# Performance work log

Hardware: AMD Instinct MI355X
Metric: run time of the kernel (lower is better)

## Reference

```python
import jax, jax.numpy as jnp
import numpy as np

EMBED_DIM = 1024
NUM_HEADS = 16
HEAD_DIM = EMBED_DIM // NUM_HEADS


def setup_inputs() -> dict:
    key = jax.random.key(0)
    ks = jax.random.split(key, 9)
    B, N, D = 2, 2048, EMBED_DIM
    s = 1.0 / np.sqrt(D)
    return {
        "x": jax.random.normal(ks[0], (B, N, D), jnp.float32),
        "Wq": jax.random.normal(ks[1], (D, D), jnp.float32) * s,
        "bq": jax.random.normal(ks[2], (D,), jnp.float32) * 0.01,
        "Wk": jax.random.normal(ks[3], (D, D), jnp.float32) * s,
        "bk": jax.random.normal(ks[4], (D,), jnp.float32) * 0.01,
        "Wv": jax.random.normal(ks[5], (D, D), jnp.float32) * s,
        "bv": jax.random.normal(ks[6], (D,), jnp.float32) * 0.01,
        "Wo": jax.random.normal(ks[7], (D, D), jnp.float32) * s,
        "bo": jax.random.normal(ks[8], (D,), jnp.float32) * 0.01,
    }


def reference(x, Wq, bq, Wk, bk, Wv, bv, Wo, bo):
    B, N, D = x.shape
    H, Hd = NUM_HEADS, HEAD_DIM
    # QKV projections (Linear: x @ W^T + b), split heads -> [B, H, N, Hd]
    q = (x @ Wq.T + bq).reshape(B, N, H, Hd).transpose(0, 2, 1, 3)
    k = (x @ Wk.T + bk).reshape(B, N, H, Hd).transpose(0, 2, 1, 3)
    v = (x @ Wv.T + bv).reshape(B, N, H, Hd).transpose(0, 2, 1, 3)
    scale = 1.0 / np.sqrt(Hd)
    scores = jnp.einsum("bhqd,bhkd->bhqk", q, k) * scale  # [B,H,N,N]
    attn = jax.nn.softmax(scores.astype(jnp.float32), axis=-1).astype(scores.dtype)
    out = jnp.einsum("bhqk,bhkd->bhqd", attn, v)  # [B,H,N,Hd]
    out = out.transpose(0, 2, 1, 3).reshape(B, N, D)
    return out @ Wo.T + bo
```

## Files before the change

kernel.cpp:

```cpp
#include <hip/hip_runtime.h>
#include <hip/hip_bf16.h>

typedef __attribute__((ext_vector_type(8))) short short8;
typedef __attribute__((ext_vector_type(4))) float f32x4;
typedef __attribute__((ext_vector_type(4))) unsigned short us4;

static __device__ __forceinline__ unsigned short f2bf(float f) {
    union { float f; unsigned u; } v; v.f = f;
    unsigned r = (v.u + 0x7FFFu + ((v.u >> 16) & 1u)) >> 16;
    return (unsigned short)r;
}
static __device__ __forceinline__ unsigned short f2bf_fast(float f) {
    union { float f; unsigned u; } v; v.f = f;
    return (unsigned short)((v.u + 0x8000u) >> 16);
}

#if __has_builtin(__builtin_amdgcn_exp2f)
#define EXP2(x) __builtin_amdgcn_exp2f(x)
#else
#define EXP2(x) exp2f(x)
#endif

static __device__ __forceinline__ void gld16(const unsigned short* g, unsigned short* l) {
    __builtin_amdgcn_global_load_lds(
        (const __attribute__((address_space(1))) void*)g,
        (__attribute__((address_space(3))) void*)l, 16, 0, 0);
}

__global__ __launch_bounds__(256) void convert_all(
    const float* __restrict__ x,  const float* __restrict__ wq,
    const float* __restrict__ wk, const float* __restrict__ wv,
    const float* __restrict__ wo, const float* __restrict__ bq,
    const float* __restrict__ bk, const float* __restrict__ bv,
    unsigned short* __restrict__ xbf, unsigned short* __restrict__ wqkv,
    unsigned short* __restrict__ wobf, float* __restrict__ bqkv)
{
    const int NX4 = (4096 * 1024) / 4;
    const int NW4 = (1024 * 1024) / 4;
    int i = blockIdx.x * 256 + threadIdx.x;
    if (i < NX4) {
        float4 v = ((const float4*)x)[i];
        us4 o = { f2bf(v.x), f2bf(v.y), f2bf(v.z), f2bf(v.w) };
        ((us4*)xbf)[i] = o;
    } else if (i < NX4 + 3 * NW4) {
        int j = i - NX4;
        const float* src = (j < NW4) ? wq + 4 * j
                         : (j < 2 * NW4) ? wk + 4 * (j - NW4)
                         : wv + 4 * (j - 2 * NW4);
        float4 v = *(const float4*)src;
        us4 o = { f2bf(v.x), f2bf(v.y), f2bf(v.z), f2bf(v.w) };
        ((us4*)wqkv)[j] = o;
    } else if (i < NX4 + 4 * NW4) {
        int j = i - NX4 - 3 * NW4;
        float4 v = ((const float4*)wo)[j];
        us4 o = { f2bf(v.x), f2bf(v.y), f2bf(v.z), f2bf(v.w) };
        ((us4*)wobf)[j] = o;
    } else if (i < NX4 + 4 * NW4 + 768) {
        int j = i - NX4 - 4 * NW4;
        const float* src = (j < 256) ? bq + 4 * j
                         : (j < 512) ? bk + 4 * (j - 256)
                         : bv + 4 * (j - 512);
        ((float4*)bqkv)[j] = *(const float4*)src;
    }
}

template <int MODE>
__global__ __launch_bounds__(256) void gemm_bt(
    const unsigned short* __restrict__ A, const unsigned short* __restrict__ B,
    const float* __restrict__ bias,
    unsigned short* __restrict__ Qb, unsigned short* __restrict__ Kb,
    unsigned short* __restrict__ Vtb, float* __restrict__ Cout, int Mtiles)
{
    __shared__ __attribute__((aligned(16))) unsigned short As[128 * 72];
    __shared__ __attribute__((aligned(16))) unsigned short Bs[128 * 72];
    const int tid = threadIdx.x, lane = tid & 63, wave = tid >> 6;
    const int bm = blockIdx.x % Mtiles, bn = blockIdx.x / Mtiles;
    const int m0 = bm * 128, n0 = bn * 128;
    const int wr = wave >> 1, wc = wave & 1;
    const int lo = lane & 15, g = lane >> 4;

    f32x4 acc[4][4];
#pragma unroll
    for (int i = 0; i < 4; ++i)
#pragma unroll
        for (int j = 0; j < 4; ++j) acc[i][j] = (f32x4){0.f, 0.f, 0.f, 0.f};

    for (int kt = 0; kt < 16; ++kt) {
        const int k0 = kt * 64;
#pragma unroll
        for (int p = 0; p < 4; ++p) {
            int idx = p * 256 + tid;
            int row = idx >> 3, c8 = (idx & 7) << 3;
            uint4 va;
            if (MODE == 0) {
                va = *(const uint4*)(A + (size_t)(m0 + row) * 1024 + k0 + c8);
            } else {
                int gr = m0 + row, b = gr >> 11, n = gr & 2047;
                va = *(const uint4*)(A + ((size_t)((b << 4) + kt) * 2048 + n) * 64 + c8);
            }
            *(uint4*)&As[row * 72 + c8] = va;
            uint4 vb = *(const uint4*)(B + (size_t)(n0 + row) * 1024 + k0 + c8);
            *(uint4*)&Bs[row * 72 + c8] = vb;
        }
        __syncthreads();
        short8 af[4][2], bf[4][2];
#pragma unroll
        for (int i = 0; i < 4; ++i)
#pragma unroll
            for (int kc = 0; kc < 2; ++kc) {
                af[i][kc] = *(const short8*)&As[(wr * 64 + i * 16 + lo) * 72 + kc * 32 + g * 8];
                bf[i][kc] = *(const short8*)&Bs[(wc * 64 + i * 16 + lo) * 72 + kc * 32 + g * 8];
            }
#pragma unroll
        for (int kc = 0; kc < 2; ++kc)
#pragma unroll
            for (int i = 0; i < 4; ++i)
#pragma unroll
                for (int j = 0; j < 4; ++j)
                    acc[i][j] = __builtin_amdgcn_mfma_f32_16x16x32_bf16(
                        af[i][kc], bf[j][kc], acc[i][j], 0, 0, 0);
        __syncthreads();
    }

#pragma unroll
    for (int i = 0; i < 4; ++i)
#pragma unroll
        for (int j = 0; j < 4; ++j)
#pragma unroll
            for (int r = 0; r < 4; ++r) {
                int gr = m0 + wr * 64 + i * 16 + g * 4 + r;
                int gc = n0 + wc * 64 + j * 16 + lo;
                float v = acc[i][j][r] + bias[gc];
                if (MODE == 0) {
                    int b = gr >> 11, n = gr & 2047;
                    int sect = gc >> 10, d = gc & 1023, h = d >> 6, hd = d & 63;
                    if (sect == 0)
                        Qb[((size_t)((b << 4) + h) * 2048 + n) * 64 + hd] = f2bf(v);
                    else if (sect == 1)
                        Kb[((size_t)((b << 4) + h) * 2048 + n) * 64 + hd] = f2bf(v);
                    else
                        Vtb[((size_t)((b << 4) + h) * 64 + hd) * 2048 + n] = f2bf(v);
                } else {
                    Cout[(size_t)gr * 1024 + gc] = v;
                }
            }
}

__global__ __launch_bounds__(256, 2) void attn_kernel(
    const unsigned short* __restrict__ Qb, const unsigned short* __restrict__ Kb,
    const unsigned short* __restrict__ Vtb, unsigned short* __restrict__ Ob)
{
    __shared__ __attribute__((aligned(16))) unsigned short Ks[128 * 64];
    __shared__ __attribute__((aligned(16))) unsigned short Vs[64 * 128];
    __shared__ __attribute__((aligned(16))) unsigned short Ps[4 * 32 * 136];
    const int tid = threadIdx.x, lane = tid & 63, wave = tid >> 6;
    const int lo = lane & 15, g = lane >> 4;
    const int bh = blockIdx.x >> 4, qt = blockIdx.x & 15;
    const size_t base = (size_t)bh * (2048 * 64);
    const int q0w = qt * 128 + wave * 32;
    const float k2 = 0.125f * 1.44269504f;

    short8 aq[2][2];
#pragma unroll
    for (int rb = 0; rb < 2; ++rb) {
        const unsigned short* qp = Qb + base + (size_t)(q0w + rb * 16 + lo) * 64 + g * 8;
        aq[rb][0] = *(const short8*)qp;
        aq[rb][1] = *(const short8*)(qp + 32);
    }
    f32x4 o[2][4];
    float l[2][4];
#pragma unroll
    for (int rb = 0; rb < 2; ++rb) {
#pragma unroll
        for (int c = 0; c < 4; ++c) o[rb][c] = (f32x4){0.f, 0.f, 0.f, 0.f};
#pragma unroll
        for (int r = 0; r < 4; ++r) l[rb][r] = 0.f;
    }
    unsigned short* myP = Ps + wave * (32 * 136);
    const unsigned short* Kg0 = Kb + base;
    const unsigned short* Vg0 = Vtb + (size_t)bh * (64 * 2048);

    for (int kt = 0; kt < 16; ++kt) {
        const int k0 = kt * 128;
#pragma unroll
        for (int i = 0; i < 4; ++i) {
            int off = (wave * 4 + i) * 512 + lane * 8;
            gld16(Kg0 + (size_t)k0 * 64 + off, &Ks[off]);
        }
#pragma unroll
        for (int i = 0; i < 4; ++i) {
            int off = (wave * 4 + i) * 512 + lane * 8;
            int row = off >> 7, col = off & 127;
            gld16(Vg0 + (size_t)row * 2048 + k0 + col, &Vs[off]);
        }
        __syncthreads();

        f32x4 s[2][8];
#pragma unroll
        for (int ct = 0; ct < 8; ++ct) {
            short8 b0 = *(const short8*)&Ks[(ct * 16 + lo) * 64 + g * 8];
            short8 b1 = *(const short8*)&Ks[(ct * 16 + lo) * 64 + 32 + g * 8];
#pragma unroll
            for (int rb = 0; rb < 2; ++rb) {
                f32x4 z = (f32x4){0.f, 0.f, 0.f, 0.f};
                s[rb][ct] = __builtin_amdgcn_mfma_f32_16x16x32_bf16(aq[rb][0], b0, z, 0, 0, 0);
                s[rb][ct] = __builtin_amdgcn_mfma_f32_16x16x32_bf16(aq[rb][1], b1, s[rb][ct], 0, 0, 0);
            }
        }
#pragma unroll
        for (int rb = 0; rb < 2; ++rb)
#pragma unroll
            for (int ct = 0; ct < 8; ++ct)
#pragma unroll
                for (int r = 0; r < 4; ++r) {
                    float p = EXP2(s[rb][ct][r] * k2);
                    l[rb][r] += p;
                    myP[(rb * 16 + g * 4 + r) * 136 + ct * 16 + lo] = f2bf_fast(p);
                }
#pragma unroll
        for (int kc = 0; kc < 4; ++kc) {
            short8 ap0 = *(const short8*)&myP[lo * 136 + kc * 32 + g * 8];
            short8 ap1 = *(const short8*)&myP[(16 + lo) * 136 + kc * 32 + g * 8];
#pragma unroll
            for (int c = 0; c < 4; ++c) {
                short8 bv = *(const short8*)&Vs[(c * 16 + lo) * 128 + kc * 32 + g * 8];
                o[0][c] = __builtin_amdgcn_mfma_f32_16x16x32_bf16(ap0, bv, o[0][c], 0, 0, 0);
                o[1][c] = __builtin_amdgcn_mfma_f32_16x16x32_bf16(ap1, bv, o[1][c], 0, 0, 0);
            }
        }
        __syncthreads();
    }

#pragma unroll
    for (int rb = 0; rb < 2; ++rb)
#pragma unroll
        for (int r = 0; r < 4; ++r) {
            float v = l[rb][r];
            v += __shfl_xor(v, 1);
            v += __shfl_xor(v, 2);
            v += __shfl_xor(v, 4);
            v += __shfl_xor(v, 8);
            l[rb][r] = 1.f / v;
        }
#pragma unroll
    for (int rb = 0; rb < 2; ++rb)
#pragma unroll
        for (int r = 0; r < 4; ++r)
#pragma unroll
            for (int c = 0; c < 4; ++c)
                Ob[base + (size_t)(q0w + rb * 16 + g * 4 + r) * 64 + c * 16 + lo] =
                    f2bf(o[rb][c][r] * l[rb][r]);
}

extern "C" void kernel_launch(void* const* d_in, const int* in_sizes, int n_in,
                              void* d_out, int out_size, void* d_ws, size_t ws_size,
                              hipStream_t stream) {
    const float* x  = (const float*)d_in[0];
    const float* Wq = (const float*)d_in[1];
    const float* bq = (const float*)d_in[2];
    const float* Wk = (const float*)d_in[3];
    const float* bk = (const float*)d_in[4];
    const float* Wv = (const float*)d_in[5];
    const float* bv = (const float*)d_in[6];
    const float* Wo = (const float*)d_in[7];
    const float* bo = (const float*)d_in[8];
    float* out = (float*)d_out;

    char* ws = (char*)d_ws;
    unsigned short* xbf  = (unsigned short*)ws;
    unsigned short* wqkv = (unsigned short*)(ws + 8388608);
    unsigned short* wobf = (unsigned short*)(ws + 14680064);
    float*          bqkv = (float*)(ws + 16777216);
    unsigned short* Qb   = (unsigned short*)(ws + 16789504);
    unsigned short* Kb   = (unsigned short*)(ws + 16789504 + 8388608);
    unsigned short* Vtb  = (unsigned short*)(ws + 16789504 + 2 * 8388608);
    unsigned short* Ob   = (unsigned short*)(ws + 16789504 + 3 * 8388608);

    convert_all<<<8195, 256, 0, stream>>>(x, Wq, Wk, Wv, Wo, bq, bk, bv,
                                          xbf, wqkv, wobf, bqkv);
    gemm_bt<0><<<32 * 24, 256, 0, stream>>>(xbf, wqkv, bqkv, Qb, Kb, Vtb, nullptr, 32);
    attn_kernel<<<2 * 16 * 16, 256, 0, stream>>>(Qb, Kb, Vtb, Ob);
    gemm_bt<1><<<32 * 8, 256, 0, stream>>>(Ob, wobf, bo, nullptr, nullptr, nullptr, out, 32);
}
```

Measured before the change: 246.7 us.

## Use k8-major LDS/global layouts, direct-to-LDS GEMM loads, and transposed attention MFMAs

```diff
diff --git a/kernel.cpp b/kernel.cpp
--- a/kernel.cpp
+++ b/kernel.cpp
@@ -10,9 +10,15 @@
     unsigned r = (v.u + 0x7FFFu + ((v.u >> 16) & 1u)) >> 16;
     return (unsigned short)r;
 }
-static __device__ __forceinline__ unsigned short f2bf_fast(float f) {
-    union { float f; unsigned u; } v; v.f = f;
-    return (unsigned short)((v.u + 0x8000u) >> 16);
+static __device__ __forceinline__ unsigned pk2(float a, float b) {
+    union { float f; unsigned u; } x, y; x.f = a; y.f = b;
+    unsigned lo = (x.u + 0x7FFFu + ((x.u >> 16) & 1u)) >> 16;
+    unsigned hi = (y.u + 0x7FFFu + ((y.u >> 16) & 1u)) >> 16;
+    return lo | (hi << 16);
+}
+static __device__ __forceinline__ unsigned pk2f(float a, float b) {
+    union { float f; unsigned u; } x, y; x.f = a; y.f = b;
+    return ((x.u + 0x8000u) >> 16) | ((y.u + 0x8000u) & 0xFFFF0000u);
 }
 
 #if __has_builtin(__builtin_amdgcn_exp2f)
@@ -26,6 +32,8 @@
         (const __attribute__((address_space(1))) void*)g,
         (__attribute__((address_space(3))) void*)l, 16, 0, 0);
 }
+
+#define QSCALE (0.125f * 1.44269504f)
 
 __global__ __launch_bounds__(256) void convert_all(
     const float* __restrict__ x,  const float* __restrict__ wq,
@@ -71,8 +79,8 @@
     unsigned short* __restrict__ Qb, unsigned short* __restrict__ Kb,
     unsigned short* __restrict__ Vtb, float* __restrict__ Cout, int Mtiles)
 {
-    __shared__ __attribute__((aligned(16))) unsigned short As[128 * 72];
-    __shared__ __attribute__((aligned(16))) unsigned short Bs[128 * 72];
+    __shared__ __attribute__((aligned(16))) unsigned short As[8192];
+    __shared__ __attribute__((aligned(16))) unsigned short Bs[8192];
     const int tid = threadIdx.x, lane = tid & 63, wave = tid >> 6;
     const int bm = blockIdx.x % Mtiles, bn = blockIdx.x / Mtiles;
     const int m0 = bm * 128, n0 = bn * 128;
@@ -89,18 +97,17 @@
         const int k0 = kt * 64;
 #pragma unroll
         for (int p = 0; p < 4; ++p) {
-            int idx = p * 256 + tid;
-            int row = idx >> 3, c8 = (idx & 7) << 3;
-            uint4 va;
+            int off = (p * 256 + tid) * 8;
+            int k8l = off >> 10, m = (off >> 3) & 127;
+            const unsigned short* srcA;
             if (MODE == 0) {
-                va = *(const uint4*)(A + (size_t)(m0 + row) * 1024 + k0 + c8);
+                srcA = A + (size_t)(m0 + m) * 1024 + k0 + k8l * 8;
             } else {
-                int gr = m0 + row, b = gr >> 11, n = gr & 2047;
-                va = *(const uint4*)(A + ((size_t)((b << 4) + kt) * 2048 + n) * 64 + c8);
-            }
-            *(uint4*)&As[row * 72 + c8] = va;
-            uint4 vb = *(const uint4*)(B + (size_t)(n0 + row) * 1024 + k0 + c8);
-            *(uint4*)&Bs[row * 72 + c8] = vb;
+                int gr = m0 + m, b = gr >> 11, n = gr & 2047;
+                srcA = A + ((size_t)((b << 4) + kt) * 2048 + n) * 64 + k8l * 8;
+            }
+            gld16(srcA, &As[off]);
+            gld16(B + (size_t)(n0 + m) * 1024 + k0 + k8l * 8, &Bs[off]);
         }
         __syncthreads();
         short8 af[4][2], bf[4][2];
@@ -108,8 +115,8 @@
         for (int i = 0; i < 4; ++i)
 #pragma unroll
             for (int kc = 0; kc < 2; ++kc) {
-                af[i][kc] = *(const short8*)&As[(wr * 64 + i * 16 + lo) * 72 + kc * 32 + g * 8];
-                bf[i][kc] = *(const short8*)&Bs[(wc * 64 + i * 16 + lo) * 72 + kc * 32 + g * 8];
+                af[i][kc] = *(const short8*)&As[((kc * 4 + g) * 128 + wr * 64 + i * 16 + lo) * 8];
+                bf[i][kc] = *(const short8*)&Bs[((kc * 4 + g) * 128 + wc * 64 + i * 16 + lo) * 8];
             }
 #pragma unroll
         for (int kc = 0; kc < 2; ++kc)
@@ -122,43 +129,61 @@
         __syncthreads();
     }
 
-#pragma unroll
-    for (int i = 0; i < 4; ++i)
-#pragma unroll
-        for (int j = 0; j < 4; ++j)
-#pragma unroll
-            for (int r = 0; r < 4; ++r) {
-                int gr = m0 + wr * 64 + i * 16 + g * 4 + r;
+    if (MODE == 0) {
+        const int sect = n0 >> 10;
+#pragma unroll
+        for (int i = 0; i < 4; ++i)
+#pragma unroll
+            for (int j = 0; j < 4; ++j) {
                 int gc = n0 + wc * 64 + j * 16 + lo;
-                float v = acc[i][j][r] + bias[gc];
-                if (MODE == 0) {
-                    int b = gr >> 11, n = gr & 2047;
-                    int sect = gc >> 10, d = gc & 1023, h = d >> 6, hd = d & 63;
-                    if (sect == 0)
-                        Qb[((size_t)((b << 4) + h) * 2048 + n) * 64 + hd] = f2bf(v);
-                    else if (sect == 1)
-                        Kb[((size_t)((b << 4) + h) * 2048 + n) * 64 + hd] = f2bf(v);
-                    else
-                        Vtb[((size_t)((b << 4) + h) * 64 + hd) * 2048 + n] = f2bf(v);
+                int d = gc & 1023, h = d >> 6, hd = d & 63;
+                float bv = bias[gc];
+                int nb = m0 + wr * 64 + i * 16 + g * 4;
+                int b = nb >> 11, n = nb & 2047;
+                size_t hb = (size_t)((b << 4) + h) * 131072;
+                if (sect == 0) {
+#pragma unroll
+                    for (int r = 0; r < 4; ++r)
+                        Qb[hb + (size_t)(n + r) * 64 + hd] =
+                            f2bf((acc[i][j][r] + bv) * QSCALE);
+                } else if (sect == 1) {
+#pragma unroll
+                    for (int r = 0; r < 4; ++r)
+                        Kb[hb + (size_t)(hd >> 3) * 16384 + (size_t)(n + r) * 8 + (hd & 7)] =
+                            f2bf(acc[i][j][r] + bv);
                 } else {
-                    Cout[(size_t)gr * 1024 + gc] = v;
+                    uint2 w;
+                    w.x = pk2(acc[i][j][0] + bv, acc[i][j][1] + bv);
+                    w.y = pk2(acc[i][j][2] + bv, acc[i][j][3] + bv);
+                    *(uint2*)&Vtb[hb + (size_t)(n >> 3) * 512 + (size_t)hd * 8 + (n & 7)] = w;
                 }
             }
+    } else {
+#pragma unroll
+        for (int i = 0; i < 4; ++i)
+#pragma unroll
+            for (int j = 0; j < 4; ++j)
+#pragma unroll
+                for (int r = 0; r < 4; ++r) {
+                    int gr = m0 + wr * 64 + i * 16 + g * 4 + r;
+                    int gc = n0 + wc * 64 + j * 16 + lo;
+                    Cout[(size_t)gr * 1024 + gc] = acc[i][j][r] + bias[gc];
+                }
+    }
 }
 
 __global__ __launch_bounds__(256, 2) void attn_kernel(
     const unsigned short* __restrict__ Qb, const unsigned short* __restrict__ Kb,
     const unsigned short* __restrict__ Vtb, unsigned short* __restrict__ Ob)
 {
-    __shared__ __attribute__((aligned(16))) unsigned short Ks[128 * 64];
-    __shared__ __attribute__((aligned(16))) unsigned short Vs[64 * 128];
-    __shared__ __attribute__((aligned(16))) unsigned short Ps[4 * 32 * 136];
+    __shared__ __attribute__((aligned(16))) unsigned short Ks[8192];
+    __shared__ __attribute__((aligned(16))) unsigned short Vs[8192];
+    __shared__ __attribute__((aligned(16))) unsigned short PT[4 * 32 * 136];
     const int tid = threadIdx.x, lane = tid & 63, wave = tid >> 6;
     const int lo = lane & 15, g = lane >> 4;
     const int bh = blockIdx.x >> 4, qt = blockIdx.x & 15;
-    const size_t base = (size_t)bh * (2048 * 64);
+    const size_t base = (size_t)bh * 131072;
     const int q0w = qt * 128 + wave * 32;
-    const float k2 = 0.125f * 1.44269504f;
 
     short8 aq[2][2];
 #pragma unroll
@@ -168,88 +193,72 @@
         aq[rb][1] = *(const short8*)(qp + 32);
     }
     f32x4 o[2][4];
-    float l[2][4];
-#pragma unroll
-    for (int rb = 0; rb < 2; ++rb) {
+    float l[2] = {0.f, 0.f};
+#pragma unroll
+    for (int rb = 0; rb < 2; ++rb)
 #pragma unroll
         for (int c = 0; c < 4; ++c) o[rb][c] = (f32x4){0.f, 0.f, 0.f, 0.f};
-#pragma unroll
-        for (int r = 0; r < 4; ++r) l[rb][r] = 0.f;
-    }
-    unsigned short* myP = Ps + wave * (32 * 136);
-    const unsigned short* Kg0 = Kb + base;
-    const unsigned short* Vg0 = Vtb + (size_t)bh * (64 * 2048);
+    unsigned short* myP = PT + wave * (32 * 136);
+    const unsigned short* Kg = Kb + base;
+    const unsigned short* Vg = Vtb + base;
 
     for (int kt = 0; kt < 16; ++kt) {
         const int k0 = kt * 128;
 #pragma unroll
         for (int i = 0; i < 4; ++i) {
             int off = (wave * 4 + i) * 512 + lane * 8;
-            gld16(Kg0 + (size_t)k0 * 64 + off, &Ks[off]);
-        }
-#pragma unroll
-        for (int i = 0; i < 4; ++i) {
-            int off = (wave * 4 + i) * 512 + lane * 8;
-            int row = off >> 7, col = off & 127;
-            gld16(Vg0 + (size_t)row * 2048 + k0 + col, &Vs[off]);
-        }
-        __syncthreads();
-
-        f32x4 s[2][8];
+            gld16(Kg + (size_t)(off >> 10) * 16384 + k0 * 8 + (off & 1023), &Ks[off]);
+            gld16(Vg + (size_t)k0 * 64 + off, &Vs[off]);
+        }
+        __syncthreads();
+
 #pragma unroll
         for (int ct = 0; ct < 8; ++ct) {
-            short8 b0 = *(const short8*)&Ks[(ct * 16 + lo) * 64 + g * 8];
-            short8 b1 = *(const short8*)&Ks[(ct * 16 + lo) * 64 + 32 + g * 8];
+            short8 kf0 = *(const short8*)&Ks[(size_t)g * 1024 + (ct * 16 + lo) * 8];
+            short8 kf1 = *(const short8*)&Ks[(size_t)(4 + g) * 1024 + (ct * 16 + lo) * 8];
 #pragma unroll
             for (int rb = 0; rb < 2; ++rb) {
                 f32x4 z = (f32x4){0.f, 0.f, 0.f, 0.f};
-                s[rb][ct] = __builtin_amdgcn_mfma_f32_16x16x32_bf16(aq[rb][0], b0, z, 0, 0, 0);
-                s[rb][ct] = __builtin_amdgcn_mfma_f32_16x16x32_bf16(aq[rb][1], b1, s[rb][ct], 0, 0, 0);
-            }
-        }
-#pragma unroll
-        for (int rb = 0; rb < 2; ++rb)
-#pragma unroll
-            for (int ct = 0; ct < 8; ++ct)
-#pragma unroll
-                for (int r = 0; r < 4; ++r) {
-                    float p = EXP2(s[rb][ct][r] * k2);
-                    l[rb][r] += p;
-                    myP[(rb * 16 + g * 4 + r) * 136 + ct * 16 + lo] = f2bf_fast(p);
-                }
+                f32x4 s = __builtin_amdgcn_mfma_f32_16x16x32_bf16(kf0, aq[rb][0], z, 0, 0, 0);
+                s = __builtin_amdgcn_mfma_f32_16x16x32_bf16(kf1, aq[rb][1], s, 0, 0, 0);
+                float p0 = EXP2(s[0]), p1 = EXP2(s[1]);
+                float p2 = EXP2(s[2]), p3 = EXP2(s[3]);
+                l[rb] += (p0 + p1) + (p2 + p3);
+                uint2 w; w.x = pk2f(p0, p1); w.y = pk2f(p2, p3);
+                *(uint2*)&myP[(rb * 16 + lo) * 136 + ct * 16 + g * 4] = w;
+            }
+        }
 #pragma unroll
         for (int kc = 0; kc < 4; ++kc) {
-            short8 ap0 = *(const short8*)&myP[lo * 136 + kc * 32 + g * 8];
-            short8 ap1 = *(const short8*)&myP[(16 + lo) * 136 + kc * 32 + g * 8];
+            short8 bp0 = *(const short8*)&myP[lo * 136 + kc * 32 + g * 8];
+            short8 bp1 = *(const short8*)&myP[(16 + lo) * 136 + kc * 32 + g * 8];
 #pragma unroll
             for (int c = 0; c < 4; ++c) {
-                short8 bv = *(const short8*)&Vs[(c * 16 + lo) * 128 + kc * 32 + g * 8];
-                o[0][c] = __builtin_amdgcn_mfma_f32_16x16x32_bf16(ap0, bv, o[0][c], 0, 0, 0);
-                o[1][c] = __builtin_amdgcn_mfma_f32_16x16x32_bf16(ap1, bv, o[1][c], 0, 0, 0);
-            }
-        }
-        __syncthreads();
-    }
-
+                short8 vf = *(const short8*)&Vs[(kc * 4 + g) * 512 + (c * 16 + lo) * 8];
+                o[0][c] = __builtin_amdgcn_mfma_f32_16x16x32_bf16(vf, bp0, o[0][c], 0, 0, 0);
+                o[1][c] = __builtin_amdgcn_mfma_f32_16x16x32_bf16(vf, bp1, o[1][c], 0, 0, 0);
+            }
+        }
+        __syncthreads();
+    }
+
+    float inv[2];
+#pragma unroll
+    for (int rb = 0; rb < 2; ++rb) {
+        float v = l[rb];
+        v += __shfl_xor(v, 16);
+        v += __shfl_xor(v, 32);
+        inv[rb] = 1.f / v;
+    }
 #pragma unroll
     for (int rb = 0; rb < 2; ++rb)
 #pragma unroll
-        for (int r = 0; r < 4; ++r) {
-            float v = l[rb][r];
-            v += __shfl_xor(v, 1);
-            v += __shfl_xor(v, 2);
-            v += __shfl_xor(v, 4);
-            v += __shfl_xor(v, 8);
-            l[rb][r] = 1.f / v;
-        }
-#pragma unroll
-    for (int rb = 0; rb < 2; ++rb)
-#pragma unroll
-        for (int r = 0; r < 4; ++r)
-#pragma unroll
-            for (int c = 0; c < 4; ++c)
-                Ob[base + (size_t)(q0w + rb * 16 + g * 4 + r) * 64 + c * 16 + lo] =
-                    f2bf(o[rb][c][r] * l[rb][r]);
+        for (int c = 0; c < 4; ++c) {
+            uint2 w;
+            w.x = pk2(o[rb][c][0] * inv[rb], o[rb][c][1] * inv[rb]);
+            w.y = pk2(o[rb][c][2] * inv[rb], o[rb][c][3] * inv[rb]);
+            *(uint2*)&Ob[base + (size_t)(q0w + rb * 16 + lo) * 64 + c * 16 + g * 4] = w;
+        }
 }
 
 extern "C" void kernel_launch(void* const* d_in, const int* in_sizes, int n_in,
@@ -279,6 +288,6 @@
     convert_all<<<8195, 256, 0, stream>>>(x, Wq, Wk, Wv, Wo, bq, bk, bv,
                                           xbf, wqkv, wobf, bqkv);
     gemm_bt<0><<<32 * 24, 256, 0, stream>>>(xbf, wqkv, bqkv, Qb, Kb, Vtb, nullptr, 32);
-    attn_kernel<<<2 * 16 * 16, 256, 0, stream>>>(Qb, Kb, Vtb, Ob);
+    attn_kernel<<<512, 256, 0, stream>>>(Qb, Kb, Vtb, Ob);
     gemm_bt<1><<<32 * 8, 256, 0, stream>>>(Ob, wobf, bo, nullptr, nullptr, nullptr, out, 32);
 }
```

Result: no change. 248.5 us (+0.7%).
